# Kernel optimization log

Measured on AMD Instinct MI355X. Metric: run time of the kernel, lower is better.

The kernel has to match this reference:

```python
import jax, jax.numpy as jnp
import numpy as np


def setup_inputs() -> dict:
    V, D, E = 4096, 128, 12288
    key = jax.random.key(0)
    k1, k2, k3 = jax.random.split(key, 3)
    features = jax.random.normal(k1, (V, D), dtype=jnp.float32)
    # random self-loop-free edge list
    v0 = jax.random.randint(k2, (E,), 0, V)
    off = jax.random.randint(k3, (E,), 1, V)
    v1 = (v0 + off) % V
    edges = jnp.stack([v0, v1]).astype(jnp.int32)  # [2, E]
    # manifold-style neighbor matrix: interior edges share 2 faces
    neighbor = (jnp.zeros((V, V), jnp.int32)
                .at[edges[0], edges[1]].set(2)
                .at[edges[1], edges[0]].set(2))
    return {"features": features, "edges": edges, "neighbor": neighbor}


def _collapse(features, edges, neighbor):
    """Greedy heap-order edge collapse. The heap is built once and only popped,
    so pop order == edges sorted by priority ||f[v0]||^2 + ||f[v1]||^2.
    Returns merge matrix A (f_out = A @ f_in), alive vertex mask, final count."""
    V = neighbor.shape[0]
    target = jnp.int32(V // 2)
    pri = jnp.sum(features * features, axis=1)          # [V]
    epri = pri[edges[0]] + pri[edges[1]]                # [E]
    order = jnp.argsort(epri)                           # heappop order (stable ties)
    alive0 = jnp.ones((V,), bool)
    A0 = jnp.eye(V, dtype=jnp.float32)
    cnt0 = jnp.int32(V)

    def step(carry, e):
        alive, n, A, cnt = carry
        v0 = edges[0, e]
        v1 = edges[1, e]
        do = (cnt > target) & alive[v0] & alive[v1] & (n[v0, v1] == 2)
        # merged neighbor row for v0; v1 dies
        r = (n[v0] + n[v1]).at[v0].set(0).at[v1].set(0)
        row0 = jnp.where(do, r, n[v0])
        row1 = jnp.where(do, jnp.zeros_like(r), n[v1])
        n = (n.at[v0, :].set(row0).at[:, v0].set(row0)
              .at[v1, :].set(row1).at[:, v1].set(row1))
        arow = jnp.where(do, 0.5 * (A[v0] + A[v1]), A[v0])
        A = A.at[v0].set(arow)
        alive = alive.at[v1].set(alive[v1] & jnp.logical_not(do))
        cnt = cnt - do.astype(jnp.int32)
        return (alive, n, A, cnt), None

    (alive, n, A, cnt), _ = jax.lax.scan(step, (alive0, neighbor, A0, cnt0), order)
    return A, alive, cnt


def reference(features, edges, neighbor):
    edges = edges.astype(jnp.int32)
    A, alive, cnt = _collapse(features, edges, neighbor)
    # clean_up() compacts removed vertices; under jit we mask dead rows instead
    pooled = (A @ features) * alive[:, None].astype(features.dtype)
    return pooled, alive, cnt
```

## Files before the change

### kernel.cpp

```cpp
#include <hip/hip_runtime.h>
#include <stdint.h>

#define V 4096
#define D 128
#define E 12288
#define NPAD 16384
#define HALF 8192
#define TARGET 2048
#define MAXM (V - TARGET)
#define ROWU32 256
#define CAP 16

#define WAIT_VM0   0x0F70
#define WAIT_LGKM0 0xC07F

#define WS_N      0u
#define WS_PRI    (V * ROWU32 * 4u)
#define WS_KEYS   (WS_PRI + V * 4u)
#define WS_PK     (WS_KEYS + NPAD * 8u)
#define WS_PAIRS  (WS_PK + E * 4u)
#define WS_MCOUNT (WS_PAIRS + MAXM * 4u)
#define WS_ALIVE  (WS_MCOUNT + 16u)

typedef const __attribute__((address_space(1))) unsigned* gas1_t;
typedef __attribute__((address_space(3))) unsigned* las3_t;

__device__ __forceinline__ unsigned getf(const uint4& r, int c) {
    unsigned lo = (c & 2) ? r.z : r.x;
    unsigned hi = (c & 2) ? r.w : r.y;
    return (c & 1) ? hi : lo;
}
__device__ __forceinline__ void andf(uint4& r, int c, unsigned msk) {
    if (c == 0) r.x &= msk; else if (c == 1) r.y &= msk;
    else if (c == 2) r.z &= msk; else r.w &= msk;
}

__global__ void k_scatter(const int* __restrict__ edges, unsigned* __restrict__ n32) {
    int e = blockIdx.x * 256 + threadIdx.x;
    if (e < E) {
        int a = edges[e], b = edges[E + e];
        atomicOr(&n32[a * ROWU32 + (b >> 4)], 2u << ((b & 15) * 2));
        atomicOr(&n32[b * ROWU32 + (a >> 4)], 2u << ((a & 15) * 2));
    }
}

__global__ void k_pri(const float* __restrict__ f, float* __restrict__ pri) {
    int v = blockIdx.x * 256 + threadIdx.x;
    if (v < V) {
        const float* p = f + v * D;
        float r[8];
#pragma unroll
        for (int j = 0; j < 8; j++) r[j] = __fmul_rn(p[j], p[j]);
        for (int i = 8; i < D; i += 8) {
#pragma unroll
            for (int j = 0; j < 8; j++)
                r[j] = __fadd_rn(r[j], __fmul_rn(p[i + j], p[i + j]));
        }
        float s01 = __fadd_rn(r[0], r[1]);
        float s23 = __fadd_rn(r[2], r[3]);
        float s45 = __fadd_rn(r[4], r[5]);
        float s67 = __fadd_rn(r[6], r[7]);
        pri[v] = __fadd_rn(__fadd_rn(s01, s23), __fadd_rn(s45, s67));
    }
}

__global__ void k_keys(const int* __restrict__ edges, const float* __restrict__ pri,
                       unsigned long long* __restrict__ keys) {
    int s = blockIdx.x * 256 + threadIdx.x;
    if (s < NPAD) {
        unsigned long long rec;
        if (s < E) {
            int a = edges[s], b = edges[E + s];
            float k = __fadd_rn(pri[a], pri[b]);
            rec = ((unsigned long long)__float_as_uint(k) << 32) | (unsigned)s;
        } else {
            rec = (0xFFFFFFFFull << 32) | (unsigned)s;
        }
        keys[s] = rec;
    }
}

__launch_bounds__(1024)
__global__ void k_sort2(unsigned long long* __restrict__ keys) {
    __shared__ unsigned long long srt[HALF];
    const int tid = threadIdx.x;
    unsigned long long* base = keys + blockIdx.x * HALF;
    for (int s = tid; s < HALF; s += 1024) srt[s] = base[s];
    __syncthreads();
    for (int k = 2; k <= HALF; k <<= 1) {
        for (int j = k >> 1; j >= 1; j >>= 1) {
            for (int i = tid; i < HALF; i += 1024) {
                int ixj = i ^ j;
                if (ixj > i) {
                    unsigned long long x = srt[i], y = srt[ixj];
                    bool up = ((i & k) == 0);
                    if ((x > y) == up) { srt[i] = y; srt[ixj] = x; }
                }
            }
            __syncthreads();
        }
    }
    for (int s = tid; s < HALF; s += 1024) base[s] = srt[s];
}

__launch_bounds__(64)
__global__ void k_mergepath(const unsigned long long* __restrict__ keys,
                            const int* __restrict__ edges, unsigned* __restrict__ pkG) {
    int t = blockIdx.x * 64 + threadIdx.x;
    if (t >= E / 64) return;
    const unsigned long long* A = keys;
    const unsigned long long* B = keys + HALF;
    int d = t * 64;
    int lo = d > HALF ? d - HALF : 0;
    int hi = d < HALF ? d : HALF;
    while (lo < hi) {
        int mid = (lo + hi) >> 1;
        if (A[mid] < B[d - 1 - mid]) lo = mid + 1; else hi = mid;
    }
    int ia = lo, ib = d - lo;
    for (int o = d; o < d + 64; o++) {
        bool takeA = (ib >= HALF) || (ia < HALF && A[ia] < B[ib]);
        unsigned long long r = takeA ? A[ia++] : B[ib++];
        int e = (int)(r & 0xFFFFFFFFull);
        int a = edges[e], b = edges[E + e];
        pkG[o] = ((unsigned)a << 16) | (unsigned)b;
    }
}

__launch_bounds__(64, 1)
__global__ void k_collapse(const unsigned* __restrict__ pkG, unsigned* n32,
                           unsigned* __restrict__ pairsG, int* __restrict__ mcountG,
                           uint8_t* __restrict__ aliveG, float* __restrict__ out) {
    __shared__ unsigned shRows[2 * CAP * ROWU32];
    __shared__ uint8_t  alive[V];
    __shared__ uint8_t  shV2S[V];
    __shared__ unsigned shCand[CAP];
    __shared__ unsigned shConf[CAP];
    const int lane = threadIdx.x;
    for (int v = lane; v < V; v += 64) { alive[v] = 1; shV2S[v] = 0xFF; }
    __syncthreads();

    int cnt = V, mcount = 0;
    bool done = false;

    for (int w = 0; w < E && !done; w += 64) {
        __builtin_amdgcn_s_waitcnt(WAIT_VM0);
        unsigned pkv = pkG[w + lane];
        const int a = (int)(pkv >> 16), b = (int)(pkv & 0xFFFFu);
        unsigned wv = *(volatile unsigned*)(n32 + a * ROWU32 + (b >> 4));
        unsigned fv = (wv >> ((b & 15) * 2)) & 3u;
        bool dec = !(alive[a] && alive[b]);

        while (!done) {
            if (!dec && fv != 2u) dec = true;
            unsigned long long mF = __ballot(!dec);
            if (!mF) break;
            int limit = cnt - TARGET; if (limit > CAP) limit = CAP;
            int flagged = (int)__popcll(mF);
            int nacc = flagged < limit ? flagged : limit;

            int myK = -1;
            if (!dec) {
                int rank = (int)__popcll(mF & ((1ull << lane) - 1ull));
                if (rank < limit) { myK = rank; shCand[rank] = pkv; }
            }
            if (lane < CAP) shConf[lane] = 0u;
            __syncthreads();

            __builtin_amdgcn_s_waitcnt(WAIT_VM0);
            for (int k = 0; k < nacc; k++) {
                unsigned cp = shCand[k];
                int v0 = (int)(cp >> 16), v1 = (int)(cp & 0xFFFFu);
                __builtin_amdgcn_global_load_lds(
                    (gas1_t)(n32 + v0 * ROWU32 + lane * 4),
                    (las3_t)(shRows + (2 * k) * ROWU32), 16, 0, 0);
                __builtin_amdgcn_global_load_lds(
                    (gas1_t)(n32 + v1 * ROWU32 + lane * 4),
                    (las3_t)(shRows + (2 * k + 1) * ROWU32), 16, 0, 0);
            }
            __builtin_amdgcn_s_waitcnt(WAIT_VM0);
            __syncthreads();

            for (int pp = lane; pp < CAP * CAP; pp += 64) {
                int k = pp >> 4, j = pp & 15;
                if (j < k && k < nacc) {
                    unsigned cj = shCand[j], ck = shCand[k];
                    int v0j = (int)(cj >> 16), v1j = (int)(cj & 0xFFFFu);
                    int v0k = (int)(ck >> 16), v1k = (int)(ck & 0xFFFFu);
                    bool c = (v0k == v0j) || (v0k == v1j) || (v1k == v0j) || (v1k == v1j);
                    c |= ((shRows[(2*j+1)*ROWU32 + (v0k >> 4)] >> ((v0k & 15)*2)) & 3u) != 0u;
                    c |= ((shRows[(2*j+1)*ROWU32 + (v1k >> 4)] >> ((v1k & 15)*2)) & 3u) != 0u;
                    c |= ((shRows[(2*k+1)*ROWU32 + (v0j >> 4)] >> ((v0j & 15)*2)) & 3u) != 0u;
                    if (c) atomicOr(&shConf[k], 1u << j);
                }
            }
            __syncthreads();

            unsigned kept = 0u;
            for (int k = 0; k < nacc; k++)
                if (shConf[k] == 0u) kept |= 1u << k;
            int nk = __popc(kept);
            if (myK >= 0 && ((kept >> myK) & 1u)) dec = true;

            if (lane < nacc && ((kept >> lane) & 1u)) {
                unsigned cp = shCand[lane];
                int v0 = (int)(cp >> 16), v1 = (int)(cp & 0xFFFFu);
                alive[v1] = 0;
                shV2S[v0] = (uint8_t)(2 * lane);
                int r = __popc(kept & ((1u << lane) - 1u));
                pairsG[mcount + r] = cp;
            }
            mcount += nk; cnt -= nk;
            __syncthreads();

            {
                int g = lane >> 2, sub = lane & 3;
                if (g < nacc && ((kept >> g) & 1u)) {
                    unsigned cp = shCand[g];
                    int v0 = (int)(cp >> 16), v1 = (int)(cp & 0xFFFFu);
                    const uint4* rowA = (const uint4*)(shRows + (2 * g) * ROWU32);
                    const uint4* rowB = (const uint4*)(shRows + (2 * g + 1) * ROWU32);
                    int m0u = v0 >> 6, m1u = v1 >> 6;
                    int sh0 = (v0 & 15) * 2, wi0 = v0 >> 4;
                    for (int t = 0; t < 16; t++) {
                        int u = sub * 16 + ((t + lane) & 15);
                        uint4 ra = rowA[u], rb = rowB[u];
                        uint4 rr;
                        rr.x = ra.x | rb.x | ((ra.x & rb.x & 0xAAAAAAAAu) >> 1);
                        rr.y = ra.y | rb.y | ((ra.y & rb.y & 0xAAAAAAAAu) >> 1);
                        rr.z = ra.z | rb.z | ((ra.z & rb.z & 0xAAAAAAAAu) >> 1);
                        rr.w = ra.w | rb.w | ((ra.w & rb.w & 0xAAAAAAAAu) >> 1);
                        if (u == m0u) andf(rr, (v0 >> 4) & 3, ~(3u << ((v0 & 15) * 2)));
                        if (u == m1u) andf(rr, (v1 >> 4) & 3, ~(3u << ((v1 & 15) * 2)));
                        ((uint4*)(n32 + v0 * ROWU32))[u] = rr;
                        ((uint4*)shRows)[(2 * g) * (ROWU32 / 4) + u] = rr;
#pragma unroll
                        for (int c = 0; c < 4; c++) {
                            unsigned bb = getf(rb, c);
                            if (!bb) continue;
                            unsigned aa = getf(ra, c), vvv = getf(rr, c);
                            int xbase = (u << 6) + (c << 4);
                            unsigned tt = bb;
                            while (tt) {
                                int q = (__ffs(tt) - 1) >> 1;
                                tt &= ~(3u << (q * 2));
                                int x = xbase + q;
                                if (x != v0 && x != v1) {
                                    unsigned dx =
                                        (((aa >> (q*2)) ^ (vvv >> (q*2))) & 3u) << sh0;
                                    if (dx) atomicXor(n32 + x * ROWU32 + wi0, dx);
                                }
                            }
                        }
                    }
                }
            }
            __syncthreads();

            if (!dec) {
                if (!alive[a] || !alive[b]) dec = true;
                else {
                    int s = shV2S[a];
                    if (s != 0xFF)
                        fv = (shRows[s * ROWU32 + (b >> 4)] >> ((b & 15) * 2)) & 3u;
                    else {
                        s = shV2S[b];
                        if (s != 0xFF)
                            fv = (shRows[s * ROWU32 + (a >> 4)] >> ((a & 15) * 2)) & 3u;
                    }
                }
            }
            __syncthreads();

            if (lane < nacc && ((kept >> lane) & 1u))
                shV2S[(int)(shCand[lane] >> 16)] = 0xFF;

            if (cnt == TARGET) done = true;
        }
    }

    for (int v = lane; v < V; v += 64) {
        uint8_t ao = alive[v];
        aliveG[v] = ao;
        out[V * D + v] = ao ? 1.0f : 0.0f;
    }
    if (lane == 0) { mcountG[0] = mcount; out[V * D + V] = (float)cnt; }
}

__launch_bounds__(256)
__global__ void k_apply(const float* __restrict__ f, const unsigned* __restrict__ pairsG,
                        const int* __restrict__ mcountG, float* __restrict__ out) {
    __shared__ unsigned pl[MAXM];
    __shared__ int rootL[256];
    __shared__ float wL[256];
    const int tid = threadIdx.x;
    const int mc = mcountG[0];
    for (int j = tid; j < mc; j += 256) pl[j] = pairsG[j];
    __syncthreads();
    int cur = blockIdx.x * 256 + tid;
    float w = 1.0f;
    for (int j = 0; j < mc; j++) {
        unsigned p = pl[j];
        int v0 = (int)(p >> 16), v1 = (int)(p & 0xFFFFu);
        if (cur == v1) { cur = v0; w *= 0.5f; }
        else if (cur == v0) w *= 0.5f;
    }
    rootL[tid] = cur;
    wL[tid] = w;
    __syncthreads();
    const int sub = tid >> 7;
    const int d = tid & 127;
    for (int s = 0; s < 256; s += 2) {
        int idx = s + sub;
        int vv = blockIdx.x * 256 + idx;
        atomicAdd(&out[rootL[idx] * D + d], wL[idx] * f[vv * D + d]);
    }
}

extern "C" void kernel_launch(void* const* d_in, const int* in_sizes, int n_in,
                              void* d_out, int out_size, void* d_ws, size_t ws_size,
                              hipStream_t stream) {
    (void)in_sizes; (void)n_in; (void)out_size; (void)ws_size;
    const float* features = (const float*)d_in[0];
    const int* edges = (const int*)d_in[1];
    uint8_t* ws = (uint8_t*)d_ws;
    unsigned* n32 = (unsigned*)(ws + WS_N);
    float* pri = (float*)(ws + WS_PRI);
    unsigned long long* keys = (unsigned long long*)(ws + WS_KEYS);
    unsigned* pkG = (unsigned*)(ws + WS_PK);
    unsigned* pairsG = (unsigned*)(ws + WS_PAIRS);
    int* mcountG = (int*)(ws + WS_MCOUNT);
    uint8_t* aliveG = ws + WS_ALIVE;
    float* out = (float*)d_out;

    hipMemsetAsync(n32, 0, (size_t)V * ROWU32 * 4, stream);
    hipMemsetAsync(out, 0, (size_t)V * D * sizeof(float), stream);
    k_pri<<<(V + 255) / 256, 256, 0, stream>>>(features, pri);
    k_scatter<<<(E + 255) / 256, 256, 0, stream>>>(edges, n32);
    k_keys<<<(NPAD + 255) / 256, 256, 0, stream>>>(edges, pri, keys);
    k_sort2<<<2, 1024, 0, stream>>>(keys);
    k_mergepath<<<(E / 64 + 63) / 64, 64, 0, stream>>>(keys, edges, pkG);
    k_collapse<<<1, 64, 0, stream>>>(pkG, n32, pairsG, mcountG, aliveG, out);
    k_apply<<<V / 256, 256, 0, stream>>>(features, pairsG, mcountG, out);
}
```

Measured before the change: 3.244 ms.

## Cache neighbor rows in a persistent LDS slot pool across collapse batches

Replaces the per-batch reload of both endpoint rows with a 48-slot LDS cache of neighbor-matrix rows that stays resident across batches. Slots are tagged by vertex, filled only on a miss with deduplicated fetches, and kept coherent by mirroring the global atomicXor updates into any cached copy. Edge-flag lookups for a new window of edges are served from the cache when possible, so the global load and its wait are skipped. The cost is more bookkeeping, extra LDS atomics and syncs, and a larger shared-memory footprint, with some risk of coherence errors.

```diff
diff --git a/kernel.cpp b/kernel.cpp
--- a/kernel.cpp
+++ b/kernel.cpp
@@ -10,6 +10,7 @@
 #define MAXM (V - TARGET)
 #define ROWU32 256
 #define CAP 16
+#define NS 48
 
 #define WAIT_VM0   0x0F70
 #define WAIT_LGKM0 0xC07F
@@ -131,25 +132,48 @@
 __global__ void k_collapse(const unsigned* __restrict__ pkG, unsigned* n32,
                            unsigned* __restrict__ pairsG, int* __restrict__ mcountG,
                            uint8_t* __restrict__ aliveG, float* __restrict__ out) {
-    __shared__ unsigned shRows[2 * CAP * ROWU32];
+    __shared__ unsigned shRows[NS * ROWU32];
     __shared__ uint8_t  alive[V];
     __shared__ uint8_t  shV2S[V];
+    __shared__ unsigned shSlotV[NS];
     __shared__ unsigned shCand[CAP];
     __shared__ unsigned shConf[CAP];
+    __shared__ uint8_t  shCS[2 * CAP];
+    __shared__ unsigned shEV[2 * CAP];
+    __shared__ unsigned shFetch[2 * CAP];
+    __shared__ unsigned long long shPinned;
     const int lane = threadIdx.x;
     for (int v = lane; v < V; v += 64) { alive[v] = 1; shV2S[v] = 0xFF; }
+    if (lane < NS) shSlotV[lane] = 0xFFFFFFFFu;
     __syncthreads();
 
     int cnt = V, mcount = 0;
     bool done = false;
 
     for (int w = 0; w < E && !done; w += 64) {
-        __builtin_amdgcn_s_waitcnt(WAIT_VM0);
         unsigned pkv = pkG[w + lane];
         const int a = (int)(pkv >> 16), b = (int)(pkv & 0xFFFFu);
-        unsigned wv = *(volatile unsigned*)(n32 + a * ROWU32 + (b >> 4));
-        unsigned fv = (wv >> ((b & 15) * 2)) & 3u;
         bool dec = !(alive[a] && alive[b]);
+        unsigned fv = 0u;
+        bool needG = false;
+        if (!dec) {
+            int s = shV2S[a];
+            if (s < NS && shSlotV[s] == (unsigned)a)
+                fv = (shRows[s * ROWU32 + (b >> 4)] >> ((b & 15) * 2)) & 3u;
+            else {
+                s = shV2S[b];
+                if (s < NS && shSlotV[s] == (unsigned)b)
+                    fv = (shRows[s * ROWU32 + (a >> 4)] >> ((a & 15) * 2)) & 3u;
+                else needG = true;
+            }
+        }
+        if (__ballot(needG)) {
+            __builtin_amdgcn_s_waitcnt(WAIT_VM0);
+            if (needG) {
+                unsigned wv = *(volatile unsigned*)(n32 + a * ROWU32 + (b >> 4));
+                fv = (wv >> ((b & 15) * 2)) & 3u;
+            }
+        }
 
         while (!done) {
             if (!dec && fv != 2u) dec = true;
@@ -165,20 +189,54 @@
                 if (rank < limit) { myK = rank; shCand[rank] = pkv; }
             }
             if (lane < CAP) shConf[lane] = 0u;
-            __syncthreads();
-
-            __builtin_amdgcn_s_waitcnt(WAIT_VM0);
-            for (int k = 0; k < nacc; k++) {
-                unsigned cp = shCand[k];
-                int v0 = (int)(cp >> 16), v1 = (int)(cp & 0xFFFFu);
-                __builtin_amdgcn_global_load_lds(
-                    (gas1_t)(n32 + v0 * ROWU32 + lane * 4),
-                    (las3_t)(shRows + (2 * k) * ROWU32), 16, 0, 0);
-                __builtin_amdgcn_global_load_lds(
-                    (gas1_t)(n32 + v1 * ROWU32 + lane * 4),
-                    (las3_t)(shRows + (2 * k + 1) * ROWU32), 16, 0, 0);
-            }
-            __builtin_amdgcn_s_waitcnt(WAIT_VM0);
+            if (lane == 0) shPinned = 0ull;
+            __syncthreads();
+
+            int ev = -1; bool isMiss = false;
+            if (lane < 2 * nacc) {
+                unsigned cp = shCand[lane >> 1];
+                ev = (lane & 1) ? (int)(cp & 0xFFFFu) : (int)(cp >> 16);
+                int s = shV2S[ev];
+                if (s < NS && shSlotV[s] == (unsigned)ev) {
+                    shCS[lane] = (uint8_t)s;
+                    atomicOr(&shPinned, 1ull << s);
+                    shEV[lane] = 0xFFFFFFFFu;
+                } else { isMiss = true; shEV[lane] = (unsigned)ev; }
+            }
+            __syncthreads();
+
+            bool leader = false;
+            if (isMiss) {
+                leader = true;
+                for (int q = 0; q < lane; q++)
+                    if (shEV[q] == (unsigned)ev) { leader = false; break; }
+            }
+            unsigned long long mLead = __ballot(leader);
+            int nf = (int)__popcll(mLead);
+            if (leader) {
+                int r = (int)__popcll(mLead & ((1ull << lane) - 1ull));
+                unsigned long long freeM = ~shPinned & ((1ull << NS) - 1ull);
+                for (int t = 0; t < r; t++) freeM &= freeM - 1ull;
+                int slot = __ffsll((long long)freeM) - 1;
+                shSlotV[slot] = (unsigned)ev;
+                shV2S[ev] = (uint8_t)slot;
+                shCS[lane] = (uint8_t)slot;
+                shFetch[r] = ((unsigned)slot << 16) | (unsigned)ev;
+            }
+            __syncthreads();
+            if (isMiss && !leader) shCS[lane] = shV2S[ev];
+
+            if (nf > 0) {
+                __builtin_amdgcn_s_waitcnt(WAIT_VM0);
+                for (int f = 0; f < nf; f++) {
+                    unsigned fe = shFetch[f];
+                    int slot = (int)(fe >> 16), vv = (int)(fe & 0xFFFFu);
+                    __builtin_amdgcn_global_load_lds(
+                        (gas1_t)(n32 + vv * ROWU32 + lane * 4),
+                        (las3_t)(shRows + slot * ROWU32), 16, 0, 0);
+                }
+                __builtin_amdgcn_s_waitcnt(WAIT_VM0);
+            }
             __syncthreads();
 
             for (int pp = lane; pp < CAP * CAP; pp += 64) {
@@ -188,9 +246,11 @@
                     int v0j = (int)(cj >> 16), v1j = (int)(cj & 0xFFFFu);
                     int v0k = (int)(ck >> 16), v1k = (int)(ck & 0xFFFFu);
                     bool c = (v0k == v0j) || (v0k == v1j) || (v1k == v0j) || (v1k == v1j);
-                    c |= ((shRows[(2*j+1)*ROWU32 + (v0k >> 4)] >> ((v0k & 15)*2)) & 3u) != 0u;
-                    c |= ((shRows[(2*j+1)*ROWU32 + (v1k >> 4)] >> ((v1k & 15)*2)) & 3u) != 0u;
-                    c |= ((shRows[(2*k+1)*ROWU32 + (v0j >> 4)] >> ((v0j & 15)*2)) & 3u) != 0u;
+                    const unsigned* rBj = shRows + (int)shCS[2 * j + 1] * ROWU32;
+                    const unsigned* rBk = shRows + (int)shCS[2 * k + 1] * ROWU32;
+                    c |= ((rBj[v0k >> 4] >> ((v0k & 15) * 2)) & 3u) != 0u;
+                    c |= ((rBj[v1k >> 4] >> ((v1k & 15) * 2)) & 3u) != 0u;
+                    c |= ((rBk[v0j >> 4] >> ((v0j & 15) * 2)) & 3u) != 0u;
                     if (c) atomicOr(&shConf[k], 1u << j);
                 }
             }
@@ -204,9 +264,7 @@
 
             if (lane < nacc && ((kept >> lane) & 1u)) {
                 unsigned cp = shCand[lane];
-                int v0 = (int)(cp >> 16), v1 = (int)(cp & 0xFFFFu);
-                alive[v1] = 0;
-                shV2S[v0] = (uint8_t)(2 * lane);
+                alive[(int)(cp & 0xFFFFu)] = 0;
                 int r = __popc(kept & ((1u << lane) - 1u));
                 pairsG[mcount + r] = cp;
             }
@@ -218,8 +276,10 @@
                 if (g < nacc && ((kept >> g) & 1u)) {
                     unsigned cp = shCand[g];
                     int v0 = (int)(cp >> 16), v1 = (int)(cp & 0xFFFFu);
-                    const uint4* rowA = (const uint4*)(shRows + (2 * g) * ROWU32);
-                    const uint4* rowB = (const uint4*)(shRows + (2 * g + 1) * ROWU32);
+                    int sA = shCS[2 * g], sB = shCS[2 * g + 1];
+                    uint4* rowA = (uint4*)(shRows + sA * ROWU32);
+                    const uint4* rowB = (const uint4*)(shRows + sB * ROWU32);
+                    if (sub == 0) shSlotV[sB] = 0xFFFFFFFFu;
                     int m0u = v0 >> 6, m1u = v1 >> 6;
                     int sh0 = (v0 & 15) * 2, wi0 = v0 >> 4;
                     for (int t = 0; t < 16; t++) {
@@ -233,7 +293,7 @@
                         if (u == m0u) andf(rr, (v0 >> 4) & 3, ~(3u << ((v0 & 15) * 2)));
                         if (u == m1u) andf(rr, (v1 >> 4) & 3, ~(3u << ((v1 & 15) * 2)));
                         ((uint4*)(n32 + v0 * ROWU32))[u] = rr;
-                        ((uint4*)shRows)[(2 * g) * (ROWU32 / 4) + u] = rr;
+                        rowA[u] = rr;
 #pragma unroll
                         for (int c = 0; c < 4; c++) {
                             unsigned bb = getf(rb, c);
@@ -248,7 +308,12 @@
                                 if (x != v0 && x != v1) {
                                     unsigned dx =
                                         (((aa >> (q*2)) ^ (vvv >> (q*2))) & 3u) << sh0;
-                                    if (dx) atomicXor(n32 + x * ROWU32 + wi0, dx);
+                                    if (dx) {
+                                        atomicXor(n32 + x * ROWU32 + wi0, dx);
+                                        int sx = shV2S[x];
+                                        if (sx < NS && shSlotV[sx] == (unsigned)x)
+                                            atomicXor(&shRows[sx * ROWU32 + wi0], dx);
+                                    }
                                 }
                             }
                         }
@@ -261,19 +326,16 @@
                 if (!alive[a] || !alive[b]) dec = true;
                 else {
                     int s = shV2S[a];
-                    if (s != 0xFF)
+                    if (s < NS && shSlotV[s] == (unsigned)a)
                         fv = (shRows[s * ROWU32 + (b >> 4)] >> ((b & 15) * 2)) & 3u;
                     else {
                         s = shV2S[b];
-                        if (s != 0xFF)
+                        if (s < NS && shSlotV[s] == (unsigned)b)
                             fv = (shRows[s * ROWU32 + (a >> 4)] >> ((a & 15) * 2)) & 3u;
                     }
                 }
             }
             __syncthreads();
-
-            if (lane < nacc && ((kept >> lane) & 1u))
-                shV2S[(int)(shCand[lane] >> 16)] = 0xFF;
 
             if (cnt == TARGET) done = true;
         }
```

New measurement: 4.493 ms. 1.39x slower.

## Use a sliding candidate window with compaction and larger conflict-free batches

Applied to the files above, without the earlier changes.

Replaces the fixed 64-edge windows with a compacting sliding window: edges still undecided shift to the front lanes via shuffles, and new edges are pulled in to refill the window. Each batch can now hold up to 32 candidate merges. Conflict resolution becomes greedy and order-aware, so edges killed by an earlier kept merge are marked decided. Neighbor-face values are cached and only reloaded when an edge touches a merged vertex. The goal is fewer serial batch iterations and barriers, at the cost of more shared memory, a more complex selection rule, and a greater risk of diverging from the sequential semantics.

```diff
diff --git a/kernel.cpp b/kernel.cpp
--- a/kernel.cpp
+++ b/kernel.cpp
@@ -9,10 +9,9 @@
 #define TARGET 2048
 #define MAXM (V - TARGET)
 #define ROWU32 256
-#define CAP 16
+#define CAP 32
 
 #define WAIT_VM0   0x0F70
-#define WAIT_LGKM0 0xC07F
 
 #define WS_N      0u
 #define WS_PRI    (V * ROWU32 * 4u)
@@ -133,28 +132,37 @@
                            uint8_t* __restrict__ aliveG, float* __restrict__ out) {
     __shared__ unsigned shRows[2 * CAP * ROWU32];
     __shared__ uint8_t  alive[V];
-    __shared__ uint8_t  shV2S[V];
     __shared__ unsigned shCand[CAP];
     __shared__ unsigned shConf[CAP];
+    __shared__ unsigned shDeadM[CAP];
     const int lane = threadIdx.x;
-    for (int v = lane; v < V; v += 64) { alive[v] = 1; shV2S[v] = 0xFF; }
+    for (int v = lane; v < V; v += 64) alive[v] = 1;
     __syncthreads();
 
-    int cnt = V, mcount = 0;
-    bool done = false;
-
-    for (int w = 0; w < E && !done; w += 64) {
-        __builtin_amdgcn_s_waitcnt(WAIT_VM0);
-        unsigned pkv = pkG[w + lane];
+    int cnt = V, mcount = 0, head = 64;
+    unsigned pkv = pkG[lane];
+    unsigned fv = 0u;
+    bool fknown = false;
+    bool dec = false;
+
+    while (true) {
         const int a = (int)(pkv >> 16), b = (int)(pkv & 0xFFFFu);
-        unsigned wv = *(volatile unsigned*)(n32 + a * ROWU32 + (b >> 4));
-        unsigned fv = (wv >> ((b & 15) * 2)) & 3u;
-        bool dec = !(alive[a] && alive[b]);
-
-        while (!done) {
-            if (!dec && fv != 2u) dec = true;
-            unsigned long long mF = __ballot(!dec);
-            if (!mF) break;
+        if (!dec && !(alive[a] && alive[b])) dec = true;
+        bool unk = !dec && !fknown;
+        bool drained = false;
+        if (__ballot(unk)) {
+            __builtin_amdgcn_s_waitcnt(WAIT_VM0);
+            drained = true;
+            if (unk) {
+                unsigned wv = *(volatile unsigned*)(n32 + a * ROWU32 + (b >> 4));
+                fv = (wv >> ((b & 15) * 2)) & 3u;
+                fknown = true;
+            }
+        }
+        if (!dec && fv != 2u) dec = true;
+        unsigned long long mF = __ballot(!dec);
+
+        if (mF) {
             int limit = cnt - TARGET; if (limit > CAP) limit = CAP;
             int flagged = (int)__popcll(mF);
             int nacc = flagged < limit ? flagged : limit;
@@ -164,10 +172,10 @@
                 int rank = (int)__popcll(mF & ((1ull << lane) - 1ull));
                 if (rank < limit) { myK = rank; shCand[rank] = pkv; }
             }
-            if (lane < CAP) shConf[lane] = 0u;
-            __syncthreads();
-
-            __builtin_amdgcn_s_waitcnt(WAIT_VM0);
+            if (lane < CAP) { shConf[lane] = 0u; shDeadM[lane] = 0u; }
+            __syncthreads();
+
+            if (!drained) __builtin_amdgcn_s_waitcnt(WAIT_VM0);
             for (int k = 0; k < nacc; k++) {
                 unsigned cp = shCand[k];
                 int v0 = (int)(cp >> 16), v1 = (int)(cp & 0xFFFFu);
@@ -182,39 +190,46 @@
             __syncthreads();
 
             for (int pp = lane; pp < CAP * CAP; pp += 64) {
-                int k = pp >> 4, j = pp & 15;
+                int k = pp >> 5, j = pp & 31;
                 if (j < k && k < nacc) {
                     unsigned cj = shCand[j], ck = shCand[k];
                     int v0j = (int)(cj >> 16), v1j = (int)(cj & 0xFFFFu);
                     int v0k = (int)(ck >> 16), v1k = (int)(ck & 0xFFFFu);
-                    bool c = (v0k == v0j) || (v0k == v1j) || (v1k == v0j) || (v1k == v1j);
-                    c |= ((shRows[(2*j+1)*ROWU32 + (v0k >> 4)] >> ((v0k & 15)*2)) & 3u) != 0u;
-                    c |= ((shRows[(2*j+1)*ROWU32 + (v1k >> 4)] >> ((v1k & 15)*2)) & 3u) != 0u;
-                    c |= ((shRows[(2*k+1)*ROWU32 + (v0j >> 4)] >> ((v0j & 15)*2)) & 3u) != 0u;
+                    bool dkill = (v0k == v1j) || (v1k == v1j);
+                    bool c = dkill || (v0k == v0j) || (v1k == v0j);
+                    const unsigned* rBj = shRows + (2 * j + 1) * ROWU32;
+                    const unsigned* rBk = shRows + (2 * k + 1) * ROWU32;
+                    c |= ((rBj[v0k >> 4] >> ((v0k & 15) * 2)) & 3u) != 0u;
+                    c |= ((rBj[v1k >> 4] >> ((v1k & 15) * 2)) & 3u) != 0u;
+                    c |= ((rBk[v0j >> 4] >> ((v0j & 15) * 2)) & 3u) != 0u;
                     if (c) atomicOr(&shConf[k], 1u << j);
+                    if (dkill) atomicOr(&shDeadM[k], 1u << j);
                 }
             }
             __syncthreads();
 
-            unsigned kept = 0u;
-            for (int k = 0; k < nacc; k++)
-                if (shConf[k] == 0u) kept |= 1u << k;
+            unsigned kept = 0u, blocked = 0u, deadm = 0u;
+            for (int k = 0; k < nacc; k++) {
+                unsigned bit = 1u << k;
+                if (shDeadM[k] & kept) { deadm |= bit; continue; }
+                if (shConf[k] & (kept | blocked)) { blocked |= bit; continue; }
+                kept |= bit;
+            }
             int nk = __popc(kept);
-            if (myK >= 0 && ((kept >> myK) & 1u)) dec = true;
+            if (myK >= 0 && (((kept | deadm) >> myK) & 1u)) dec = true;
 
             if (lane < nacc && ((kept >> lane) & 1u)) {
                 unsigned cp = shCand[lane];
-                int v0 = (int)(cp >> 16), v1 = (int)(cp & 0xFFFFu);
-                alive[v1] = 0;
-                shV2S[v0] = (uint8_t)(2 * lane);
+                alive[(int)(cp & 0xFFFFu)] = 0;
                 int r = __popc(kept & ((1u << lane) - 1u));
                 pairsG[mcount + r] = cp;
             }
             mcount += nk; cnt -= nk;
             __syncthreads();
+            if (cnt == TARGET) break;
 
             {
-                int g = lane >> 2, sub = lane & 3;
+                int g = lane >> 1, sub = lane & 1;
                 if (g < nacc && ((kept >> g) & 1u)) {
                     unsigned cp = shCand[g];
                     int v0 = (int)(cp >> 16), v1 = (int)(cp & 0xFFFFu);
@@ -222,8 +237,8 @@
                     const uint4* rowB = (const uint4*)(shRows + (2 * g + 1) * ROWU32);
                     int m0u = v0 >> 6, m1u = v1 >> 6;
                     int sh0 = (v0 & 15) * 2, wi0 = v0 >> 4;
-                    for (int t = 0; t < 16; t++) {
-                        int u = sub * 16 + ((t + lane) & 15);
+                    for (int t = 0; t < 32; t++) {
+                        int u = sub * 32 + ((t + lane) & 31);
                         uint4 ra = rowA[u], rb = rowB[u];
                         uint4 rr;
                         rr.x = ra.x | rb.x | ((ra.x & rb.x & 0xAAAAAAAAu) >> 1);
@@ -233,7 +248,6 @@
                         if (u == m0u) andf(rr, (v0 >> 4) & 3, ~(3u << ((v0 & 15) * 2)));
                         if (u == m1u) andf(rr, (v1 >> 4) & 3, ~(3u << ((v1 & 15) * 2)));
                         ((uint4*)(n32 + v0 * ROWU32))[u] = rr;
-                        ((uint4*)shRows)[(2 * g) * (ROWU32 / 4) + u] = rr;
 #pragma unroll
                         for (int c = 0; c < 4; c++) {
                             unsigned bb = getf(rb, c);
@@ -257,25 +271,41 @@
             }
             __syncthreads();
 
-            if (!dec) {
-                if (!alive[a] || !alive[b]) dec = true;
-                else {
-                    int s = shV2S[a];
-                    if (s != 0xFF)
-                        fv = (shRows[s * ROWU32 + (b >> 4)] >> ((b & 15) * 2)) & 3u;
-                    else {
-                        s = shV2S[b];
-                        if (s != 0xFF)
-                            fv = (shRows[s * ROWU32 + (a >> 4)] >> ((a & 15) * 2)) & 3u;
-                    }
+            if (!dec && fknown) {
+                unsigned km = kept;
+                while (km) {
+                    int j = __ffs(km) - 1; km &= km - 1u;
+                    int v0j = (int)(shCand[j] >> 16);
+                    if (a == v0j || b == v0j) { fknown = false; break; }
                 }
             }
             __syncthreads();
-
-            if (lane < nacc && ((kept >> lane) & 1u))
-                shV2S[(int)(shCand[lane] >> 16)] = 0xFF;
-
-            if (cnt == TARGET) done = true;
+        } else {
+            if (head >= E) break;
+        }
+
+        {
+            unsigned long long mU = __ballot(!dec);
+            int nU = (int)__popcll(mU);
+            int p = 0;
+#pragma unroll
+            for (int step = 32; step; step >>= 1) {
+                int cand = p + step;
+                unsigned long long pref =
+                    (cand >= 64) ? ~0ull : ((1ull << cand) - 1ull);
+                if ((int)__popcll(mU & pref) <= lane) p = cand;
+            }
+            unsigned npkv = (unsigned)__shfl((int)pkv, p);
+            unsigned nfv  = (unsigned)__shfl((int)fv, p);
+            int      nfk  = __shfl((int)fknown, p);
+            if (lane < nU) {
+                pkv = npkv; fv = nfv; fknown = (nfk != 0); dec = false;
+            } else {
+                int idx = head + lane - nU;
+                if (idx < E) { pkv = pkG[idx]; fknown = false; dec = false; }
+                else dec = true;
+            }
+            head += 64 - nU;
         }
     }
 
```

New measurement: 3.818 ms. 17.7% more time.

## Cache candidate neighbor rows in persistent LDS slots and reuse across rounds

Applied to the files above, without the earlier changes.

Gives each pending candidate edge a persistent LDS slot that holds its two neighbor rows. A slot is reloaded only when a committed merge touches its vertices, instead of refetching every candidate's rows from global memory each round. The conflict resolution becomes a sequential greedy pass that also records candidates killed by an earlier kept merge, and the face-count read is deferred until it is needed. This saves global-to-LDS traffic and allows more merges per round, but adds slot bookkeeping with wave shuffles and staleness checks whose correctness is subtle.

```diff
diff --git a/kernel.cpp b/kernel.cpp
--- a/kernel.cpp
+++ b/kernel.cpp
@@ -10,9 +10,9 @@
 #define MAXM (V - TARGET)
 #define ROWU32 256
 #define CAP 16
+#define NPAIR 16
 
 #define WAIT_VM0   0x0F70
-#define WAIT_LGKM0 0xC07F
 
 #define WS_N      0u
 #define WS_PRI    (V * ROWU32 * 4u)
@@ -33,6 +33,11 @@
 __device__ __forceinline__ void andf(uint4& r, int c, unsigned msk) {
     if (c == 0) r.x &= msk; else if (c == 1) r.y &= msk;
     else if (c == 2) r.z &= msk; else r.w &= msk;
+}
+__device__ __forceinline__ unsigned wave_or32(unsigned v) {
+#pragma unroll
+    for (int o = 32; o; o >>= 1) v |= (unsigned)__shfl_xor((int)v, o);
+    return v;
 }
 
 __global__ void k_scatter(const int* __restrict__ edges, unsigned* __restrict__ n32) {
@@ -131,54 +136,109 @@
 __global__ void k_collapse(const unsigned* __restrict__ pkG, unsigned* n32,
                            unsigned* __restrict__ pairsG, int* __restrict__ mcountG,
                            uint8_t* __restrict__ aliveG, float* __restrict__ out) {
-    __shared__ unsigned shRows[2 * CAP * ROWU32];
+    __shared__ unsigned shRows[2 * NPAIR * ROWU32];
     __shared__ uint8_t  alive[V];
-    __shared__ uint8_t  shV2S[V];
     __shared__ unsigned shCand[CAP];
     __shared__ unsigned shConf[CAP];
+    __shared__ unsigned shDeadM[CAP];
+    __shared__ uint8_t  shCS[2 * CAP];
     const int lane = threadIdx.x;
-    for (int v = lane; v < V; v += 64) { alive[v] = 1; shV2S[v] = 0xFF; }
+    for (int v = lane; v < V; v += 64) alive[v] = 1;
     __syncthreads();
 
     int cnt = V, mcount = 0;
     bool done = false;
+    unsigned freeMask = 0xFFFFu;
+    bool hasSlot = false, rowsStale = false;
+    int ownPair = 0;
 
     for (int w = 0; w < E && !done; w += 64) {
-        __builtin_amdgcn_s_waitcnt(WAIT_VM0);
         unsigned pkv = pkG[w + lane];
         const int a = (int)(pkv >> 16), b = (int)(pkv & 0xFFFFu);
-        unsigned wv = *(volatile unsigned*)(n32 + a * ROWU32 + (b >> 4));
-        unsigned fv = (wv >> ((b & 15) * 2)) & 3u;
         bool dec = !(alive[a] && alive[b]);
+        bool fvKnown = false;
+        unsigned fv = 0u;
 
         while (!done) {
+            bool needF = !dec && !fvKnown;
+            if (__ballot(needF)) {
+                __builtin_amdgcn_s_waitcnt(WAIT_VM0);
+                if (needF) {
+                    unsigned wv = *(volatile unsigned*)(n32 + a * ROWU32 + (b >> 4));
+                    fv = (wv >> ((b & 15) * 2)) & 3u;
+                    fvKnown = true;
+                }
+            }
             if (!dec && fv != 2u) dec = true;
+
+            {
+                unsigned fb = (dec && hasSlot) ? (1u << ownPair) : 0u;
+                fb = wave_or32(fb);
+                freeMask |= fb;
+                if (dec) hasSlot = false;
+            }
+
             unsigned long long mF = __ballot(!dec);
             if (!mF) break;
+
             int limit = cnt - TARGET; if (limit > CAP) limit = CAP;
-            int flagged = (int)__popcll(mF);
-            int nacc = flagged < limit ? flagged : limit;
-
-            int myK = -1;
-            if (!dec) {
-                int rank = (int)__popcll(mF & ((1ull << lane) - 1ull));
-                if (rank < limit) { myK = rank; shCand[rank] = pkv; }
-            }
-            if (lane < CAP) shConf[lane] = 0u;
-            __syncthreads();
-
-            __builtin_amdgcn_s_waitcnt(WAIT_VM0);
-            for (int k = 0; k < nacc; k++) {
-                unsigned cp = shCand[k];
-                int v0 = (int)(cp >> 16), v1 = (int)(cp & 0xFFFFu);
-                __builtin_amdgcn_global_load_lds(
-                    (gas1_t)(n32 + v0 * ROWU32 + lane * 4),
-                    (las3_t)(shRows + (2 * k) * ROWU32), 16, 0, 0);
-                __builtin_amdgcn_global_load_lds(
-                    (gas1_t)(n32 + v1 * ROWU32 + lane * 4),
-                    (las3_t)(shRows + (2 * k + 1) * ROWU32), 16, 0, 0);
-            }
-            __builtin_amdgcn_s_waitcnt(WAIT_VM0);
+            const unsigned long long below = (1ull << lane) - 1ull;
+            int rank = (int)__popcll(mF & below);
+            bool sel0 = !dec && (rank < limit);
+
+            bool needClaim = sel0 && !hasSlot;
+            for (int attempt = 0; attempt < 2; attempt++) {
+                unsigned long long cm = __ballot(needClaim);
+                if (!cm) break;
+                int ci = (int)__popcll(cm & below);
+                int avail = __popc(freeMask);
+                unsigned cb = 0u;
+                if (needClaim && ci < avail) {
+                    unsigned t = freeMask;
+                    for (int q = 0; q < ci; q++) t &= t - 1u;
+                    ownPair = __ffs(t) - 1;
+                    hasSlot = true; rowsStale = true; needClaim = false;
+                    cb = 1u << ownPair;
+                }
+                cb = wave_or32(cb);
+                freeMask &= ~cb;
+                if (__ballot(needClaim)) {
+                    unsigned fb = (!sel0 && hasSlot) ? (1u << ownPair) : 0u;
+                    fb = wave_or32(fb);
+                    freeMask |= fb;
+                    if (!sel0 && hasSlot) hasSlot = false;
+                } else break;
+            }
+            bool sel = sel0 && hasSlot;
+            unsigned long long selm = __ballot(sel);
+            int nacc = (int)__popcll(selm);
+            int myK = sel ? (int)__popcll(selm & below) : -1;
+            if (sel) {
+                shCand[myK] = pkv;
+                shCS[2 * myK] = (uint8_t)(2 * ownPair);
+                shCS[2 * myK + 1] = (uint8_t)(2 * ownPair + 1);
+            }
+            if (lane < CAP) { shConf[lane] = 0u; shDeadM[lane] = 0u; }
+
+            unsigned long long fm2 = __ballot(sel && rowsStale);
+            if (fm2) {
+                __builtin_amdgcn_s_waitcnt(WAIT_VM0);
+                unsigned long long t = fm2;
+                while (t) {
+                    int l = __ffsll((long long)t) - 1; t &= t - 1ull;
+                    int aL = __shfl(a, l);
+                    int bL = __shfl(b, l);
+                    int pr = __shfl(ownPair, l);
+                    __builtin_amdgcn_global_load_lds(
+                        (gas1_t)(n32 + aL * ROWU32 + lane * 4),
+                        (las3_t)(shRows + (2 * pr) * ROWU32), 16, 0, 0);
+                    __builtin_amdgcn_global_load_lds(
+                        (gas1_t)(n32 + bL * ROWU32 + lane * 4),
+                        (las3_t)(shRows + (2 * pr + 1) * ROWU32), 16, 0, 0);
+                }
+                __builtin_amdgcn_s_waitcnt(WAIT_VM0);
+                if (sel) rowsStale = false;
+            }
             __syncthreads();
 
             for (int pp = lane; pp < CAP * CAP; pp += 64) {
@@ -187,39 +247,45 @@
                     unsigned cj = shCand[j], ck = shCand[k];
                     int v0j = (int)(cj >> 16), v1j = (int)(cj & 0xFFFFu);
                     int v0k = (int)(ck >> 16), v1k = (int)(ck & 0xFFFFu);
-                    bool c = (v0k == v0j) || (v0k == v1j) || (v1k == v0j) || (v1k == v1j);
-                    c |= ((shRows[(2*j+1)*ROWU32 + (v0k >> 4)] >> ((v0k & 15)*2)) & 3u) != 0u;
-                    c |= ((shRows[(2*j+1)*ROWU32 + (v1k >> 4)] >> ((v1k & 15)*2)) & 3u) != 0u;
-                    c |= ((shRows[(2*k+1)*ROWU32 + (v0j >> 4)] >> ((v0j & 15)*2)) & 3u) != 0u;
+                    bool dkill = (v0k == v1j) || (v1k == v1j);
+                    bool c = dkill || (v0k == v0j) || (v1k == v0j);
+                    const unsigned* rBj = shRows + (int)shCS[2 * j + 1] * ROWU32;
+                    const unsigned* rBk = shRows + (int)shCS[2 * k + 1] * ROWU32;
+                    c |= ((rBj[v0k >> 4] >> ((v0k & 15) * 2)) & 3u) != 0u;
+                    c |= ((rBj[v1k >> 4] >> ((v1k & 15) * 2)) & 3u) != 0u;
+                    c |= ((rBk[v0j >> 4] >> ((v0j & 15) * 2)) & 3u) != 0u;
                     if (c) atomicOr(&shConf[k], 1u << j);
-                }
-            }
-            __syncthreads();
-
-            unsigned kept = 0u;
-            for (int k = 0; k < nacc; k++)
-                if (shConf[k] == 0u) kept |= 1u << k;
+                    if (dkill) atomicOr(&shDeadM[k], 1u << j);
+                }
+            }
+            __syncthreads();
+
+            unsigned kept = 0u, blocked = 0u, deadm = 0u;
+            for (int k = 0; k < nacc; k++) {
+                unsigned bit = 1u << k;
+                if (shDeadM[k] & kept) { deadm |= bit; continue; }
+                if (shConf[k] & (kept | blocked)) { blocked |= bit; continue; }
+                kept |= bit;
+            }
             int nk = __popc(kept);
-            if (myK >= 0 && ((kept >> myK) & 1u)) dec = true;
-
-            if (lane < nacc && ((kept >> lane) & 1u)) {
-                unsigned cp = shCand[lane];
-                int v0 = (int)(cp >> 16), v1 = (int)(cp & 0xFFFFu);
-                alive[v1] = 0;
-                shV2S[v0] = (uint8_t)(2 * lane);
-                int r = __popc(kept & ((1u << lane) - 1u));
-                pairsG[mcount + r] = cp;
+            if (myK >= 0 && (((kept | deadm) >> myK) & 1u)) dec = true;
+
+            if (myK >= 0 && ((kept >> myK) & 1u)) {
+                alive[b] = 0;
+                int r = __popc(kept & ((1u << myK) - 1u));
+                pairsG[mcount + r] = pkv;
             }
             mcount += nk; cnt -= nk;
             __syncthreads();
+            if (cnt == TARGET) { done = true; break; }
 
             {
                 int g = lane >> 2, sub = lane & 3;
                 if (g < nacc && ((kept >> g) & 1u)) {
                     unsigned cp = shCand[g];
                     int v0 = (int)(cp >> 16), v1 = (int)(cp & 0xFFFFu);
-                    const uint4* rowA = (const uint4*)(shRows + (2 * g) * ROWU32);
-                    const uint4* rowB = (const uint4*)(shRows + (2 * g + 1) * ROWU32);
+                    const uint4* rowA = (const uint4*)(shRows + (int)shCS[2*g] * ROWU32);
+                    const uint4* rowB = (const uint4*)(shRows + (int)shCS[2*g+1] * ROWU32);
                     int m0u = v0 >> 6, m1u = v1 >> 6;
                     int sh0 = (v0 & 15) * 2, wi0 = v0 >> 4;
                     for (int t = 0; t < 16; t++) {
@@ -233,7 +299,6 @@
                         if (u == m0u) andf(rr, (v0 >> 4) & 3, ~(3u << ((v0 & 15) * 2)));
                         if (u == m1u) andf(rr, (v1 >> 4) & 3, ~(3u << ((v1 & 15) * 2)));
                         ((uint4*)(n32 + v0 * ROWU32))[u] = rr;
-                        ((uint4*)shRows)[(2 * g) * (ROWU32 / 4) + u] = rr;
 #pragma unroll
                         for (int c = 0; c < 4; c++) {
                             unsigned bb = getf(rb, c);
@@ -257,25 +322,29 @@
             }
             __syncthreads();
 
-            if (!dec) {
-                if (!alive[a] || !alive[b]) dec = true;
-                else {
-                    int s = shV2S[a];
-                    if (s != 0xFF)
-                        fv = (shRows[s * ROWU32 + (b >> 4)] >> ((b & 15) * 2)) & 3u;
-                    else {
-                        s = shV2S[b];
-                        if (s != 0xFF)
-                            fv = (shRows[s * ROWU32 + (a >> 4)] >> ((a & 15) * 2)) & 3u;
+            {
+                unsigned km = kept;
+                while (km) {
+                    int k2 = __ffs(km) - 1; km &= km - 1u;
+                    unsigned cp = shCand[k2];
+                    int v0k = (int)(cp >> 16), v1k = (int)(cp & 0xFFFFu);
+                    if (!dec) {
+                        if (a == v0k || b == v0k) fvKnown = false;
+                        if (hasSlot && !rowsStale) {
+                            if (a == v0k || b == v0k || a == v1k || b == v1k)
+                                rowsStale = true;
+                            else {
+                                unsigned f1 = (shRows[(2*ownPair)*ROWU32 + (v1k>>4)]
+                                               >> ((v1k & 15) * 2)) & 3u;
+                                unsigned f2 = (shRows[(2*ownPair+1)*ROWU32 + (v1k>>4)]
+                                               >> ((v1k & 15) * 2)) & 3u;
+                                if (f1 | f2) rowsStale = true;
+                            }
+                        }
                     }
                 }
             }
             __syncthreads();
-
-            if (lane < nacc && ((kept >> lane) & 1u))
-                shV2S[(int)(shCand[lane] >> 16)] = 0xFF;
-
-            if (cnt == TARGET) done = true;
         }
     }
 
```

After: 3.757 ms. +15.8%, slower.
